# Kernel tuning notes

Measured on AMD Instinct MI355X. Metric: run time of the kernel, lower is better.

Reference implementation:

```python
import itertools
import jax, jax.numpy as jnp
import numpy as np

N = 1024


def _static(n):
    # Static (trace-time) index/mask structures, identical to the torch module.
    rail_shape = (2, 2, n + 1, n + 1)
    im = np.zeros(rail_shape, dtype=bool)
    im[0, :, 1:, 1:] = True
    im[1, :, :-1, :-1] = True
    om = np.zeros(rail_shape, dtype=bool)
    om[0, :, :-1, :-1] = True
    om[1, :, 1:, 1:] = True
    # 8 bit patterns over the 3 leave-one-out inputs -> (8, 3)
    bits = np.asarray(list(itertools.product(range(2), repeat=3)), dtype=np.float32)
    in_idx = np.nonzero(im.reshape(-1))[0]   # 4*n*n gather indices
    out_idx = np.nonzero(om.reshape(-1))[0]  # 4*n*n scatter indices
    return in_idx, out_idx, bits


def setup_inputs() -> dict:
    key = jax.random.key(0)
    k1, k2, k3 = jax.random.split(key, 3)
    n = N
    rail_len = 4 * (n + 1) ** 2
    return {
        "x": jax.random.uniform(k1, (n,), jnp.float32),
        "toggle_gates": jax.random.normal(k2, (4, 8, n, n), jnp.float32),
        "rail_state": jax.random.uniform(k3, (rail_len,), jnp.float32),
        "mask": jnp.ones((rail_len,), jnp.int32),
    }


def reference(x, toggle_gates, rail_state, mask):
    n = toggle_gates.shape[-1]
    in_idx, out_idx, bits = _static(n)

    # Write input x into rail_state[1, 1, :len(x), 0] (view write in torch).
    rail = rail_state.reshape(2, 2, n + 1, n + 1)
    rail = rail.at[1, 1, : x.shape[0], 0].set(x).reshape(-1)

    # Gather the 4 input planes: (4, n, n)
    new_inputs = rail[in_idx].reshape(4, n, n)
    tw = jax.nn.sigmoid(toggle_gates)  # (4, 8, n, n)

    bits_b = jnp.asarray(bits)[:, :, None, None]  # (8, 3, 1, 1)
    others = np.array([[j for j in range(4) if j != i] for i in range(4)])

    outs = []
    for i in range(4):  # fixed small loop over the 4 rail directions
        inp_i = new_inputs[others[i]]  # (3, n, n) leave-one-out inputs
        # soft AND over bit patterns: (8, n, n)
        w = jnp.prod(1.0 - jnp.abs(bits_b - inp_i[None]), axis=1)
        toggled = tw[i] * new_inputs[i] + (1.0 - tw[i]) * (1.0 - new_inputs[i])
        outs.append((toggled * w).sum(0))  # (n, n)

    new_out = jnp.clip(jnp.stack(outs).reshape(-1), 0.0, 1.0)
    rail = rail.at[out_idx].set(new_out)

    # mask is all-ones, so rail[mask] == rail; multiply keeps shape static.
    return rail * mask.astype(rail.dtype) * toggle_gates.reshape(-1)[0]
```

## Files before the change

kernel.cpp:

```cpp
#include <hip/hip_runtime.h>


constexpr int N     = 1024;
constexpr int NP1   = N + 1;
constexpr int PLANE = NP1 * NP1;
constexpr int NN    = N * N;

typedef float floatx4 __attribute__((ext_vector_type(4)));

__device__ __forceinline__ float sigmoidf_fast(float t) {
    return __builtin_amdgcn_rcpf(1.0f + __expf(-t));
}

__global__ __launch_bounds__(256, 5) void asic_fused(
    const float* __restrict__ x,
    const float* __restrict__ tg,
    const float* __restrict__ rail,
    const int*  __restrict__ mask,
    float* __restrict__ out)
{
    const int tid  = blockIdx.x * 256 + threadIdx.x;
    const float g0 = tg[0];

    {
        const int per = 2 * N + 1;
        if (tid < 4 * per) {
            const int plane = tid / per;
            const int k = tid % per;
            int r, c;
            if (plane < 2) {
                if (k <= N) { r = N; c = k; }
                else        { r = k - (N + 1); c = N; }
            } else {
                if (k <= N) { r = 0; c = k; }
                else        { r = k - N; c = 0; }
            }
            const int flat = plane * PLANE + r * NP1 + c;
            float v = (plane == 3 && c == 0 && r < N) ? x[r] : rail[flat];
            out[flat] = v * (float)mask[flat] * g0;
        }
    }

    const int pix0 = tid << 2;
    const int r    = pix0 >> 10;
    const int c0   = pix0 & (N - 1);

    float u[4][4];
    const int b01 = (r + 1) * NP1 + (c0 + 1);
    const int b23 = r * NP1 + c0;
#pragma unroll
    for (int q = 0; q < 4; ++q) {
        u[0][q] = rail[0 * PLANE + b01 + q];
        u[1][q] = rail[1 * PLANE + b01 + q];
        u[2][q] = rail[2 * PLANE + b23 + q];
        u[3][q] = rail[3 * PLANE + b23 + q];
    }
    if (c0 == 0) u[3][0] = x[r];

#pragma unroll
    for (int i = 0; i < 4; ++i) {
        const int o0 = (i == 0) ? 1 : 0;
        const int o1 = (i <= 1) ? 2 : 1;
        const int o2 = (i <= 2) ? 3 : 2;

        float A0[4], A1[4], B0[4], B1[4], C0[4], C1[4];
#pragma unroll
        for (int q = 0; q < 4; ++q) {
            A0[q] = 1.0f - fabsf(u[o0][q]);  A1[q] = 1.0f - fabsf(1.0f - u[o0][q]);
            B0[q] = 1.0f - fabsf(u[o1][q]);  B1[q] = 1.0f - fabsf(1.0f - u[o1][q]);
            C0[q] = 1.0f - fabsf(u[o2][q]);  C1[q] = 1.0f - fabsf(1.0f - u[o2][q]);
        }

        float s0[4] = {0.f, 0.f, 0.f, 0.f};
        float s1[4] = {0.f, 0.f, 0.f, 0.f};
#pragma unroll
        for (int p = 0; p < 8; ++p) {
            const floatx4 tv = __builtin_nontemporal_load(
                reinterpret_cast<const floatx4*>(&tg[(i * 8 + p) * NN + pix0]));
            const float tw[4] = { sigmoidf_fast(tv.x), sigmoidf_fast(tv.y),
                                  sigmoidf_fast(tv.z), sigmoidf_fast(tv.w) };
            const int b0 = p >> 2, b1 = (p >> 1) & 1, b2 = p & 1;
#pragma unroll
            for (int q = 0; q < 4; ++q) {
                const float w = (b0 ? A1[q] : A0[q]) *
                                (b1 ? B1[q] : B0[q]) *
                                (b2 ? C1[q] : C0[q]);
                s0[q] += w;
                s1[q]  = fmaf(tw[q], w, s1[q]);
            }
        }

#pragma unroll
        for (int q = 0; q < 4; ++q) {
            const float A = 2.0f * u[i][q] - 1.0f;
            const float B = 1.0f - u[i][q];
            float acc = fmaf(A, s1[q], B * s0[q]);
            acc = fminf(fmaxf(acc, 0.0f), 1.0f);
            const int flat = (i < 2) ? (i * PLANE + r * NP1 + (c0 + q))
                                     : (i * PLANE + (r + 1) * NP1 + (c0 + q + 1));
            __builtin_nontemporal_store(acc * (float)mask[flat] * g0, &out[flat]);
        }
    }
}

extern "C" void kernel_launch(void* const* d_in, const int* in_sizes, int n_in,
                              void* d_out, int out_size, void* d_ws, size_t ws_size,
                              hipStream_t stream) {
    const float* x    = (const float*)d_in[0];
    const float* tg   = (const float*)d_in[1];
    const float* rail = (const float*)d_in[2];
    const int*   mask = (const int*)d_in[3];
    float* out = (float*)d_out;

    asic_fused<<<(NN / 4) / 256, 256, 0, stream>>>(x, tg, rail, mask, out);
}
```

Measured before the change: 225.2 us.

## Factor soft-AND weighted sum algebraically and batch gate loads per direction

New measurement: 220.2 us. 1.02x faster.

```diff
diff --git a/kernel.cpp b/kernel.cpp
--- a/kernel.cpp
+++ b/kernel.cpp
@@ -63,42 +63,47 @@
         const int o1 = (i <= 1) ? 2 : 1;
         const int o2 = (i <= 2) ? 3 : 2;
 
-        float A0[4], A1[4], B0[4], B1[4], C0[4], C1[4];
-#pragma unroll
-        for (int q = 0; q < 4; ++q) {
-            A0[q] = 1.0f - fabsf(u[o0][q]);  A1[q] = 1.0f - fabsf(1.0f - u[o0][q]);
-            B0[q] = 1.0f - fabsf(u[o1][q]);  B1[q] = 1.0f - fabsf(1.0f - u[o1][q]);
-            C0[q] = 1.0f - fabsf(u[o2][q]);  C1[q] = 1.0f - fabsf(1.0f - u[o2][q]);
-        }
-
-        float s0[4] = {0.f, 0.f, 0.f, 0.f};
-        float s1[4] = {0.f, 0.f, 0.f, 0.f};
+        floatx4 tv[8];
 #pragma unroll
         for (int p = 0; p < 8; ++p) {
-            const floatx4 tv = __builtin_nontemporal_load(
+            tv[p] = __builtin_nontemporal_load(
                 reinterpret_cast<const floatx4*>(&tg[(i * 8 + p) * NN + pix0]));
-            const float tw[4] = { sigmoidf_fast(tv.x), sigmoidf_fast(tv.y),
-                                  sigmoidf_fast(tv.z), sigmoidf_fast(tv.w) };
-            const int b0 = p >> 2, b1 = (p >> 1) & 1, b2 = p & 1;
-#pragma unroll
-            for (int q = 0; q < 4; ++q) {
-                const float w = (b0 ? A1[q] : A0[q]) *
-                                (b1 ? B1[q] : B0[q]) *
-                                (b2 ? C1[q] : C0[q]);
-                s0[q] += w;
-                s1[q]  = fmaf(tw[q], w, s1[q]);
-            }
         }
 
 #pragma unroll
         for (int q = 0; q < 4; ++q) {
+            const float a0 = 1.0f - fabsf(u[o0][q]);
+            const float a1 = 1.0f - fabsf(1.0f - u[o0][q]);
+            const float b0 = 1.0f - fabsf(u[o1][q]);
+            const float b1 = 1.0f - fabsf(1.0f - u[o1][q]);
+            const float cc0 = 1.0f - fabsf(u[o2][q]);
+            const float cc1 = 1.0f - fabsf(1.0f - u[o2][q]);
+
+            const float s0 = (a0 + a1) * (b0 + b1) * (cc0 + cc1);
+
+            const float tw0 = sigmoidf_fast(tv[0][q]);
+            const float tw1 = sigmoidf_fast(tv[1][q]);
+            const float tw2 = sigmoidf_fast(tv[2][q]);
+            const float tw3 = sigmoidf_fast(tv[3][q]);
+            const float tw4 = sigmoidf_fast(tv[4][q]);
+            const float tw5 = sigmoidf_fast(tv[5][q]);
+            const float tw6 = sigmoidf_fast(tv[6][q]);
+            const float tw7 = sigmoidf_fast(tv[7][q]);
+            const float d00 = fmaf(tw1, cc1, tw0 * cc0);
+            const float d01 = fmaf(tw3, cc1, tw2 * cc0);
+            const float d10 = fmaf(tw5, cc1, tw4 * cc0);
+            const float d11 = fmaf(tw7, cc1, tw6 * cc0);
+            const float e0  = fmaf(b1, d01, b0 * d00);
+            const float e1  = fmaf(b1, d11, b0 * d10);
+            const float s1  = fmaf(a1, e1, a0 * e0);
+
             const float A = 2.0f * u[i][q] - 1.0f;
             const float B = 1.0f - u[i][q];
-            float acc = fmaf(A, s1[q], B * s0[q]);
+            float acc = fmaf(A, s1, B * s0);
             acc = fminf(fmaxf(acc, 0.0f), 1.0f);
             const int flat = (i < 2) ? (i * PLANE + r * NP1 + (c0 + q))
                                      : (i * PLANE + (r + 1) * NP1 + (c0 + q + 1));
-            __builtin_nontemporal_store(acc * (float)mask[flat] * g0, &out[flat]);
+            out[flat] = acc * (float)mask[flat] * g0;
         }
     }
 }
```
